# Performance work log

Measured on AMD Instinct MI355X. Metric: run time of the kernel, lower is better.

## Reference

```python
import math
import jax, jax.numpy as jnp
import numpy as np

B, N, C, H = 4, 1025, 768, 12
D = C // H                      # head_dim = 64
SCALE = D ** -0.5
NUM = N // 4                    # CSA block size = 256
FUSE_T = math.ceil(0.1 * (N - 1))     # 103
ENH_T = math.ceil(0.1 * (N - 1))      # 103


def _csa_mask():
    # has_cls=True: tokens 1..4*NUM get block id 0..3; cls (idx 0) gets -1 (unmasked).
    bid = (jnp.arange(N) - 1) // NUM
    same = (bid[:, None] == bid[None, :]) & (bid[:, None] >= 0) & (bid[:, None] < 4)
    return jnp.where(same, -jnp.inf, 0.0).astype(jnp.float32)  # [N, N]


def setup_inputs() -> dict:
    key = jax.random.key(0)
    kx, kq, kw, kb = jax.random.split(key, 4)
    x = jax.random.normal(kx, (B, N, C), dtype=jnp.float32)
    w_qkv = jax.random.normal(kq, (3 * C, C), dtype=jnp.float32) * 0.02  # Linear(C, 3C, bias=False)
    w_out = jax.random.normal(kw, (C, C), dtype=jnp.float32) * 0.02
    b_out = jax.random.normal(kb, (C,), dtype=jnp.float32) * 0.02
    return {"x": x, "w_qkv": w_qkv, "w_out": w_out, "b_out": b_out}


def reference(x, w_qkv, w_out, b_out):
    b, n, c = x.shape
    h, d = H, c // H
    # qkv projection + rearrange 'b n (qkv h d) -> qkv b h n d'
    qkv = (x @ w_qkv.T).reshape(b, n, 3, h, d).transpose(2, 0, 3, 1, 4)
    q, k, v = qkv[0], qkv[1], qkv[2]          # each [b, h, n, d]

    scores = jnp.einsum('bhxd,bhyd->bhxy', q, k) * SCALE + _csa_mask()
    att = jax.nn.softmax(scores, axis=-1)     # [b, h, n, n]  (dropout=0, eval)

    ctx = jnp.einsum('bhxy,bhyd->bhxd', att, v)
    out = ctx.transpose(0, 2, 1, 3).reshape(b, n, c) @ w_out.T + b_out

    # cls-attention-driven token selection
    cls_attn = att[:, :, 0, 1:].mean(axis=1)  # [b, n-1]
    _, fuse_idx = jax.lax.top_k(-cls_attn, FUSE_T)   # smallest, ascending
    _, enh_idx = jax.lax.top_k(cls_attn, ENH_T)      # largest, descending
    fuse_index = jnp.broadcast_to(fuse_idx[:, :, None], (b, FUSE_T, c))
    enhance_index = jnp.broadcast_to(enh_idx[:, :, None], (b, ENH_T, c))
    return (out, enhance_index, enh_idx, fuse_index, fuse_idx, cls_attn)
```

## Files before the change

kernel.cpp:

```cpp
#include <hip/hip_runtime.h>


#define B_  4
#define N_  1025
#define C_  768
#define H_  12
#define D_  64
#define M_TOT (B_ * N_)
#define M_PAD 4224
#define KEXP 2304
#define NPAD 1088

#define OFF_EIND 3148800
#define OFF_EIDX 3465216
#define OFF_FIND 3465628
#define OFF_FIDX 3782044
#define OFF_CLS  3782456

#define WS_F64   0
#define WS_XS    196608
#define WS_QKVB  5062656
#define WS_OUTB  7716864
#define WS_QE    8601600
#define WS_KE    11943936
#define WS_VT    15286272

#define DQ0 0
#define DMS 3072
#define DLG 39936
#define DMX 89136
#define DZ  89184
#define DMV 89232

#define SPLIT_A_ITEMS (M_PAD * 192)
#define SPLIT_B1_ITEMS (2304 * 192)
#define SPLIT_B2_ITEMS (768 * 192)
#define SPLIT_TOTAL (SPLIT_A_ITEMS + SPLIT_B1_ITEMS + SPLIT_B2_ITEMS)
#define SPLIT_BLOCKS ((SPLIT_TOTAL + 255) / 256)

typedef short s16x8 __attribute__((ext_vector_type(8)));
typedef float f32x4 __attribute__((ext_vector_type(4)));

__device__ inline unsigned short f2bf(float f) {
    unsigned u = __float_as_uint(f);
    u += 0x7FFF + ((u >> 16) & 1);
    return (unsigned short)(u >> 16);
}
__device__ inline float bf2f(unsigned short h) {
    return __uint_as_float(((unsigned)h) << 16);
}

__device__ __forceinline__ void gl2lds16(const unsigned short* g, unsigned short* l) {
    __builtin_amdgcn_global_load_lds(
        (const __attribute__((address_space(1))) unsigned int*)g,
        (__attribute__((address_space(3))) unsigned int*)l,
        16, 0, 0);
}

__device__ inline void gemm_decode(int lid, int NT, int& m, int& n) {
    int gi = lid / (8 * NT);
    int r  = lid % (8 * NT);
    int base = gi * 8;
    int gsize = (33 - base < 8) ? (33 - base) : 8;
    n = r / gsize;
    m = base + r % gsize;
}

__global__ __launch_bounds__(256) void fused_split_q0_kernel(
    const float* __restrict__ x, const float* __restrict__ w_qkv,
    const float* __restrict__ w_out,
    unsigned short* __restrict__ xs, unsigned short* __restrict__ qkvB,
    unsigned short* __restrict__ outB, double* __restrict__ dws)
{
    if (blockIdx.x >= SPLIT_BLOCKS) {
        const int t = threadIdx.x;
        const int wg = (blockIdx.x - SPLIT_BLOCKS) * 4 + (t >> 6);
        const int lane = t & 63;
        const int b = wg / 768, rem = wg - b * 768;
        const float* x0 = x + (size_t)b * N_ * C_;
        const float* wr = w_qkv + (size_t)rem * C_;
        double s = 0.0;
        #pragma unroll
        for (int i = 0; i < 12; i++) {
            int c = lane + i*64;
            s += (double)x0[c] * (double)wr[c];
        }
        #pragma unroll
        for (int o = 1; o < 64; o <<= 1) s += __shfl_xor(s, o);
        if (lane == 0) dws[DQ0 + wg] = s * 0.125;
        return;
    }
    int idx = blockIdx.x * 256 + threadIdx.x;
    if (idx < SPLIT_A_ITEMS) {
        int m = idx / 192, c4 = (idx - m * 192) * 4;
        ushort4 hi = make_ushort4(0,0,0,0), lo = hi;
        if (m < M_TOT) {
            float4 f = *(const float4*)&x[(size_t)m * C_ + c4];
            hi.x = f2bf(f.x); hi.y = f2bf(f.y); hi.z = f2bf(f.z); hi.w = f2bf(f.w);
            lo.x = f2bf(f.x - bf2f(hi.x)); lo.y = f2bf(f.y - bf2f(hi.y));
            lo.z = f2bf(f.z - bf2f(hi.z)); lo.w = f2bf(f.w - bf2f(hi.w));
        }
        unsigned short* d = xs + (size_t)m * KEXP + c4;
        *(ushort4*)(d)        = hi;
        *(ushort4*)(d + 768)  = hi;
        *(ushort4*)(d + 1536) = lo;
        return;
    }
    idx -= SPLIT_A_ITEMS;
    const float* src;
    unsigned short* dst;
    if (idx < SPLIT_B1_ITEMS) { src = w_qkv; dst = qkvB; }
    else { idx -= SPLIT_B1_ITEMS; if (idx >= SPLIT_B2_ITEMS) return; src = w_out; dst = outB; }
    int m = idx / 192, c4 = (idx - m * 192) * 4;
    float4 f = *(const float4*)&src[(size_t)m * C_ + c4];
    ushort4 hi, lo;
    hi.x = f2bf(f.x); hi.y = f2bf(f.y); hi.z = f2bf(f.z); hi.w = f2bf(f.w);
    lo.x = f2bf(f.x - bf2f(hi.x)); lo.y = f2bf(f.y - bf2f(hi.y));
    lo.z = f2bf(f.z - bf2f(hi.z)); lo.w = f2bf(f.w - bf2f(hi.w));
    unsigned short* d = dst + (size_t)m * KEXP + c4;
    *(ushort4*)(d)        = hi;
    *(ushort4*)(d + 768)  = lo;
    *(ushort4*)(d + 1536) = hi;
}

__global__ __launch_bounds__(256) void fused_gemm_qkv_ms_kernel(
    const unsigned short* __restrict__ A, const unsigned short* __restrict__ Bm,
    unsigned short* __restrict__ qe, unsigned short* __restrict__ ke,
    unsigned short* __restrict__ vtp,
    const float* __restrict__ w_qkv, double* __restrict__ dws)
{
    __shared__ unsigned short AsF[3*4096];
    __shared__ unsigned short BsF[3*4096];

    if (blockIdx.x >= 594) {
        double* q0s = (double*)AsF;
        const int lid = blockIdx.x - 594;
        const int cb = lid % 3;
        const int h  = (lid / 3) % 12;
        const int b  = lid / 36;
        const int t = threadIdx.x;
        const int c = cb * 256 + t;
        if (t < 64) q0s[t] = dws[DQ0 + (b*H_ + h)*64 + t];
        __syncthreads();
        const float* wk = w_qkv + (size_t)(C_ + h*64) * C_ + c;
        double s = 0.0;
        #pragma unroll 8
        for (int d = 0; d < 64; d++) s += q0s[d] * (double)wk[(size_t)d * C_];
        dws[DMS + ((size_t)(b*H_ + h))*768 + c] = s;
        return;
    }

    int mi, ni;
    gemm_decode(blockIdx.x, 18, mi, ni);
    const int n0 = ni * 128;
    const int m0 = mi * 128;
    const int t = threadIdx.x;
    const int lane = t & 63, wv = t >> 6;
    const int wr = wv >> 1, wc = wv & 1;
    const int q4 = lane >> 4, r = lane & 15;
    const int lrr = lane >> 2;
    const int lcc = ((lane & 3) ^ ((lane >> 3) & 3)) * 8;
    const int sw  = (q4 ^ ((r >> 1) & 3)) * 8;

    f32x4 acc[4][4];
    #pragma unroll
    for (int i = 0; i < 4; i++)
        #pragma unroll
        for (int j = 0; j < 4; j++)
            #pragma unroll
            for (int e = 0; e < 4; e++) acc[i][j][e] = 0.f;

    const unsigned short* gA = A  + (size_t)(m0 + wv*16 + lrr) * KEXP + lcc;
    const unsigned short* gB = Bm + (size_t)(n0 + wv*16 + lrr) * KEXP + lcc;

    auto STAGE = [&](int kt, int o) {
        const unsigned short* a = gA + kt * 32;
        const unsigned short* b = gB + kt * 32;
        gl2lds16(a,                       AsF + o + wv*512);
        gl2lds16(a + (size_t)64 * KEXP,   AsF + o + 2048 + wv*512);
        gl2lds16(b,                       BsF + o + wv*512);
        gl2lds16(b + (size_t)64 * KEXP,   BsF + o + 2048 + wv*512);
    };

    STAGE(0, 0);
    STAGE(1, 4096);

    int cb = 0;
    for (int it = 0; it < 72; ++it) {
        if (it + 1 < 72) asm volatile("s_waitcnt vmcnt(4)" ::: "memory");
        else             asm volatile("s_waitcnt vmcnt(0)" ::: "memory");
        __builtin_amdgcn_s_barrier();
        asm volatile("" ::: "memory");
        __builtin_amdgcn_sched_barrier(0);
        if (it + 2 < 72) {
            int nb = (cb >= 1) ? cb - 1 : cb + 2;
            STAGE(it + 2, nb * 4096);
        }
        const int cbuf = cb * 4096;
        s16x8 af[4], bfr[4];
        #pragma unroll
        for (int i = 0; i < 4; i++) {
            af[i]  = *(const s16x8*)&AsF[cbuf + (wr*64 + i*16 + r)*32 + sw];
            bfr[i] = *(const s16x8*)&BsF[cbuf + (wc*64 + i*16 + r)*32 + sw];
        }
        #pragma unroll
        for (int i = 0; i < 4; i++)
            #pragma unroll
            for (int j = 0; j < 4; j++)
                acc[i][j] = __builtin_amdgcn_mfma_f32_16x16x32_bf16(af[i], bfr[j], acc[i][j], 0, 0, 0);
        cb = (cb < 2) ? cb + 1 : 0;
    }

    const int sel = n0 / C_;
    const int off = n0 % C_;
    const float scl = (sel == 0) ? 0.125f : 1.0f;
    #pragma unroll
    for (int i = 0; i < 4; i++) {
        #pragma unroll
        for (int rr = 0; rr < 4; rr++) {
            int gm = m0 + wr*64 + i*16 + q4*4 + rr;
            if (gm < M_TOT) {
                int bb = gm / N_, n = gm - bb * N_;
                #pragma unroll
                for (int j = 0; j < 4; j++) {
                    int col = off + wc*64 + j*16 + r;
                    int h = col >> 6, d = col & 63;
                    float val = acc[i][j][rr] * scl;
                    unsigned short hi = f2bf(val);
                    unsigned short lo = f2bf(val - bf2f(hi));
                    size_t bh = (size_t)(bb*H_ + h);
                    if (sel <= 1) {
                        unsigned short* dst = (sel == 0 ? qe : ke) + (bh*NPAD + n)*128;
                        dst[d]      = hi;
                        dst[64 + d] = lo;
                    } else {
                        unsigned short* dst = vtp + bh*128*NPAD;
                        dst[(size_t)d*NPAD + n]        = hi;
                        dst[(size_t)(64 + d)*NPAD + n] = lo;
                    }
                }
            }
        }
    }
}

__global__ __launch_bounds__(256, 4) void fused_attn_logits_kernel(
    const unsigned short* __restrict__ qe, const unsigned short* __restrict__ ke,
    const unsigned short* __restrict__ vtp, unsigned short* __restrict__ ctxs,
    const float* __restrict__ x, double* __restrict__ dws)
{
    __shared__ unsigned short KP[64*128];
    __shared__ unsigned short VP[128*64];

    if (blockIdx.x >= 816) {
        double* xsd = (double*)KP;
        const int lid = blockIdx.x - 816;
        const int j = lid % 1025, b = lid / 1025;
        const int t = threadIdx.x;
        const int w = t >> 6, lane = t & 63;
        const float* xr = x + ((size_t)b * N_ + j) * C_;
        for (int c = t; c < C_; c += 256) xsd[c] = (double)xr[c];
        __syncthreads();
        for (int hh = 0; hh < 3; hh++) {
            int h = w + hh * 4;
            const double* ms = dws + DMS + ((size_t)(b*H_ + h))*768;
            double s = 0.0;
            #pragma unroll
            for (int i = 0; i < 12; i++) {
                int c = lane + i*64;
                s += xsd[c] * ms[c];
            }
            #pragma unroll
            for (int o = 1; o < 64; o <<= 1) s += __shfl_xor(s, o);
            if (lane == 0) dws[DLG + ((size_t)(b*H_ + h))*1025 + j] = s;
        }
        return;
    }

    const int qt = blockIdx.x / 48;
    const int g  = blockIdx.x - qt * 48;
    const int h = g % 12, b = g / 12;
    const int t = threadIdx.x;
    const int w = t >> 6, lane = t & 63;
    const int quad = lane >> 4, r16 = lane & 15;
    const size_t bh = (size_t)(b*H_ + h);

    s16x8 ah0, ah1, al0, al1;
    {
        const unsigned short* qrow = qe + (bh*NPAD + qt*64 + w*16 + r16) * 128;
        const int q8 = quad * 8;
        ah0 = *(const s16x8*)(qrow + q8);
        ah1 = *(const s16x8*)(qrow + 32 + q8);
        al0 = *(const s16x8*)(qrow + 64 + q8);
        al1 = *(const s16x8*)(qrow + 96 + q8);
    }

    int qu;
    {
        int rlo = qt*64, rhi = min(qt*64 + 63, N_ - 1);
        if (rlo == 0) qu = -2;
        else { int b1 = (rlo-1)>>8, b2 = (rhi-1)>>8; qu = (b1==b2) ? b1 : -2; }
    }

    float m_run[4], l_run[4];
    f32x4 ctx[4];
    #pragma unroll
    for (int i = 0; i < 4; i++) {
        m_run[i] = -1e30f; l_run[i] = 0.f;
        #pragma unroll
        for (int e = 0; e < 4; e++) ctx[i][e] = 0.f;
    }

    const unsigned short* keb = ke  + (bh*NPAD) * 128;
    const unsigned short* vtb = vtp + bh*(size_t)128*NPAD;

    const int kchunk = (t & 15) ^ ((t >> 4) & 15);
    const int vchunk = (t & 7)  ^ ((t >> 3) & 7);
    const unsigned short* kg0 = keb + (size_t)(t >> 4) * 128 + kchunk * 8;
    const unsigned short* vg0 = vtb + (size_t)(t >> 3) * NPAD + vchunk * 8;

    const int s0 = (quad ^ r16) << 3;
    const int sv = (quad ^ (r16 & 7)) << 3;
    unsigned short* Pew = KP + w*16*128;

    for (int kt = 0; kt < 17; kt++) {
        if (qu >= 0 && kt > 0) {
            int clo = kt*64, chi = min(kt*64 + 63, N_ - 1);
            int b1 = (clo-1)>>8, b2 = (chi-1)>>8;
            if (b1 == b2 && b1 == qu) continue;
        }

        __syncthreads();
        {
            const unsigned short* kg = kg0 + (size_t)kt * 64 * 128;
            const unsigned short* vg = vg0 + kt * 64;
            #pragma unroll
            for (int i = 0; i < 4; i++) {
                gl2lds16(kg + i * 2048,              KP + i*2048 + w*512);
                gl2lds16(vg + (size_t)i * 32 * NPAD, VP + i*2048 + w*512);
            }
        }
        __syncthreads();

        f32x4 st[4];
        #pragma unroll
        for (int j = 0; j < 4; j++)
            #pragma unroll
            for (int e = 0; e < 4; e++) st[j][e] = 0.f;
        #pragma unroll
        for (int j = 0; j < 4; j++) {
            const unsigned short* kr = &KP[(j*16 + r16) * 128];
            s16x8 bh0 = *(const s16x8*)&kr[s0];
            s16x8 bh1 = *(const s16x8*)&kr[s0 ^ 32];
            s16x8 bl0 = *(const s16x8*)&kr[s0 ^ 64];
            s16x8 bl1 = *(const s16x8*)&kr[s0 ^ 96];
            st[j] = __builtin_amdgcn_mfma_f32_16x16x32_bf16(ah0, bh0, st[j], 0,0,0);
            st[j] = __builtin_amdgcn_mfma_f32_16x16x32_bf16(ah1, bh1, st[j], 0,0,0);
            st[j] = __builtin_amdgcn_mfma_f32_16x16x32_bf16(ah0, bl0, st[j], 0,0,0);
            st[j] = __builtin_amdgcn_mfma_f32_16x16x32_bf16(ah1, bl1, st[j], 0,0,0);
            st[j] = __builtin_amdgcn_mfma_f32_16x16x32_bf16(al0, bh0, st[j], 0,0,0);
            st[j] = __builtin_amdgcn_mfma_f32_16x16x32_bf16(al1, bh1, st[j], 0,0,0);
        }

        float pv[4][4];
        float alpha[4];
        #pragma unroll
        for (int reg = 0; reg < 4; reg++) {
            int gr = qt*64 + w*16 + quad*4 + reg;
            int qb = (gr >= 1) ? ((gr - 1) >> 8) : -1;
            float mx = -1e30f;
            float vv[4];
            #pragma unroll
            for (int j = 0; j < 4; j++) {
                int gc = kt*64 + j*16 + r16;
                bool ok = (gr < N_) && (gc < N_) &&
                          !((gr >= 1) && (gc >= 1) && (((gc - 1) >> 8) == qb));
                vv[j] = ok ? st[j][reg] : -1e30f;
                mx = fmaxf(mx, vv[j]);
            }
            mx = fmaxf(mx, __shfl_xor(mx, 1));
            mx = fmaxf(mx, __shfl_xor(mx, 2));
            mx = fmaxf(mx, __shfl_xor(mx, 4));
            mx = fmaxf(mx, __shfl_xor(mx, 8));
            float mnew = fmaxf(m_run[reg], mx);
            alpha[reg] = __expf(m_run[reg] - mnew);
            m_run[reg] = mnew;
            float ps = 0.f;
            #pragma unroll
            for (int j = 0; j < 4; j++) {
                float pp = (vv[j] > -1e29f) ? __expf(vv[j] - mnew) : 0.f;
                pv[reg][j] = pp; ps += pp;
            }
            ps += __shfl_xor(ps, 1);
            ps += __shfl_xor(ps, 2);
            ps += __shfl_xor(ps, 4);
            ps += __shfl_xor(ps, 8);
            l_run[reg] = l_run[reg] * alpha[reg] + ps;
        }

        __syncthreads();

        #pragma unroll
        for (int reg = 0; reg < 4; reg++) {
            int lrow = quad*4 + reg;
            #pragma unroll
            for (int j = 0; j < 4; j++) {
                float pp = pv[reg][j];
                unsigned short ph = f2bf(pp);
                unsigned short pl = f2bf(pp - bf2f(ph));
                int colh = j*16 + r16;
                int coll = 64 + colh;
                Pew[lrow*128 + (((colh >> 3) ^ lrow) << 3) + (colh & 7)] = ph;
                Pew[lrow*128 + (((coll >> 3) ^ lrow) << 3) + (coll & 7)] = pl;
            }
        }

        #pragma unroll
        for (int nj = 0; nj < 4; nj++)
            #pragma unroll
            for (int reg = 0; reg < 4; reg++)
                ctx[nj][reg] *= alpha[reg];

        {
            const unsigned short* pr = &Pew[r16 * 128];
            s16x8 ph0 = *(const s16x8*)&pr[s0];
            s16x8 ph1 = *(const s16x8*)&pr[s0 ^ 32];
            s16x8 pl0 = *(const s16x8*)&pr[s0 ^ 64];
            s16x8 pl1 = *(const s16x8*)&pr[s0 ^ 96];
            #pragma unroll
            for (int nj = 0; nj < 4; nj++) {
                const unsigned short* vh = &VP[(nj*16 + r16) * 64];
                const unsigned short* vl = &VP[(64 + nj*16 + r16) * 64];
                s16x8 vh0 = *(const s16x8*)&vh[sv];
                s16x8 vh1 = *(const s16x8*)&vh[sv ^ 32];
                s16x8 vl0 = *(const s16x8*)&vl[sv];
                s16x8 vl1 = *(const s16x8*)&vl[sv ^ 32];
                ctx[nj] = __builtin_amdgcn_mfma_f32_16x16x32_bf16(ph0, vh0, ctx[nj], 0,0,0);
                ctx[nj] = __builtin_amdgcn_mfma_f32_16x16x32_bf16(ph1, vh1, ctx[nj], 0,0,0);
                ctx[nj] = __builtin_amdgcn_mfma_f32_16x16x32_bf16(ph0, vl0, ctx[nj], 0,0,0);
                ctx[nj] = __builtin_amdgcn_mfma_f32_16x16x32_bf16(ph1, vl1, ctx[nj], 0,0,0);
                ctx[nj] = __builtin_amdgcn_mfma_f32_16x16x32_bf16(pl0, vh0, ctx[nj], 0,0,0);
                ctx[nj] = __builtin_amdgcn_mfma_f32_16x16x32_bf16(pl1, vh1, ctx[nj], 0,0,0);
            }
        }
    }

    #pragma unroll
    for (int reg = 0; reg < 4; reg++) {
        int gr = qt*64 + w*16 + quad*4 + reg;
        if (gr < N_) {
            float inv = 1.0f / l_run[reg];
            size_t row = (size_t)(b*N_ + gr) * KEXP;
            #pragma unroll
            for (int nj = 0; nj < 4; nj++) {
                float val = ctx[nj][reg] * inv;
                unsigned short hi = f2bf(val);
                unsigned short lo = f2bf(val - bf2f(hi));
                int c = h*64 + nj*16 + r16;
                ctxs[row + c]        = hi;
                ctxs[row + 768 + c]  = hi;
                ctxs[row + 1536 + c] = lo;
            }
        }
    }
}

__global__ __launch_bounds__(256) void fused_gemm_out_reduce_kernel(
    const unsigned short* __restrict__ A, const unsigned short* __restrict__ Bm,
    const float* __restrict__ bias, float* __restrict__ out,
    double* __restrict__ dws)
{
    __shared__ unsigned short AsF[3*4096];
    __shared__ unsigned short BsF[3*4096];

    if (blockIdx.x >= 198) {
        double* red = (double*)AsF;
        const int lid = blockIdx.x - 198;
        const int h = lid % 12, b = lid / 12;
        const int t = threadIdx.x;
        const double* lg = dws + DLG + ((size_t)(b*H_ + h))*1025;
        double mloc = -1e300;
        for (int j = t; j < N_; j += 256) mloc = fmax(mloc, lg[j]);
        red[t] = mloc; __syncthreads();
        for (int o = 128; o > 0; o >>= 1) {
            if (t < o) red[t] = fmax(red[t], red[t+o]);
            __syncthreads();
        }
        double mx = red[0]; __syncthreads();
        double sloc = 0.0;
        for (int j = t; j < N_; j += 256) sloc += exp(lg[j] - mx);
        red[t] = sloc; __syncthreads();
        for (int o = 128; o > 0; o >>= 1) {
            if (t < o) red[t] += red[t+o];
            __syncthreads();
        }
        if (t == 0) {
            dws[DMX + b*H_ + h] = mx;
            dws[DZ  + b*H_ + h] = red[0];
        }
        return;
    }

    int mi, ni;
    gemm_decode(blockIdx.x, 6, mi, ni);
    const int n0 = ni * 128;
    const int m0 = mi * 128;
    const int t = threadIdx.x;
    const int lane = t & 63, wv = t >> 6;
    const int wr = wv >> 1, wc = wv & 1;
    const int q4 = lane >> 4, r = lane & 15;
    const int lrr = lane >> 2;
    const int lcc = ((lane & 3) ^ ((lane >> 3) & 3)) * 8;
    const int sw  = (q4 ^ ((r >> 1) & 3)) * 8;

    f32x4 acc[4][4];
    #pragma unroll
    for (int i = 0; i < 4; i++)
        #pragma unroll
        for (int j = 0; j < 4; j++)
            #pragma unroll
            for (int e = 0; e < 4; e++) acc[i][j][e] = 0.f;

    const unsigned short* gA = A  + (size_t)(m0 + wv*16 + lrr) * KEXP + lcc;
    const unsigned short* gB = Bm + (size_t)(n0 + wv*16 + lrr) * KEXP + lcc;

    auto STAGE = [&](int kt, int o) {
        const unsigned short* a = gA + kt * 32;
        const unsigned short* b = gB + kt * 32;
        gl2lds16(a,                       AsF + o + wv*512);
        gl2lds16(a + (size_t)64 * KEXP,   AsF + o + 2048 + wv*512);
        gl2lds16(b,                       BsF + o + wv*512);
        gl2lds16(b + (size_t)64 * KEXP,   BsF + o + 2048 + wv*512);
    };

    STAGE(0, 0);
    STAGE(1, 4096);

    int cb = 0;
    for (int it = 0; it < 72; ++it) {
        if (it + 1 < 72) asm volatile("s_waitcnt vmcnt(4)" ::: "memory");
        else             asm volatile("s_waitcnt vmcnt(0)" ::: "memory");
        __builtin_amdgcn_s_barrier();
        asm volatile("" ::: "memory");
        __builtin_amdgcn_sched_barrier(0);
        if (it + 2 < 72) {
            int nb = (cb >= 1) ? cb - 1 : cb + 2;
            STAGE(it + 2, nb * 4096);
        }
        const int cbuf = cb * 4096;
        s16x8 af[4], bfr[4];
        #pragma unroll
        for (int i = 0; i < 4; i++) {
            af[i]  = *(const s16x8*)&AsF[cbuf + (wr*64 + i*16 + r)*32 + sw];
            bfr[i] = *(const s16x8*)&BsF[cbuf + (wc*64 + i*16 + r)*32 + sw];
        }
        #pragma unroll
        for (int i = 0; i < 4; i++)
            #pragma unroll
            for (int j = 0; j < 4; j++)
                acc[i][j] = __builtin_amdgcn_mfma_f32_16x16x32_bf16(af[i], bfr[j], acc[i][j], 0, 0, 0);
        cb = (cb < 2) ? cb + 1 : 0;
    }

    #pragma unroll
    for (int i = 0; i < 4; i++) {
        #pragma unroll
        for (int rr = 0; rr < 4; rr++) {
            int gm = m0 + wr*64 + i*16 + q4*4 + rr;
            if (gm < M_TOT) {
                #pragma unroll
                for (int j = 0; j < 4; j++) {
                    int col = n0 + wc*64 + j*16 + r;
                    out[(size_t)gm * C_ + col] = acc[i][j][rr] + bias[col];
                }
            }
        }
    }
}

__global__ __launch_bounds__(256) void cls_score_kernel(
    const double* __restrict__ dwsr, double* __restrict__ dws,
    float* __restrict__ out)
{
    const int idx = blockIdx.x * 256 + threadIdx.x;
    const int b = idx >> 10, t = idx & 1023;
    double s = 0.0;
    #pragma unroll
    for (int h = 0; h < H_; h++) {
        double mx = dwsr[DMX + b*H_ + h];
        double Z  = dwsr[DZ  + b*H_ + h];
        double lg = dwsr[DLG + ((size_t)(b*H_ + h))*1025 + (t + 1)];
        s += exp(lg - mx) / Z;
    }
    s *= (1.0 / 12.0);
    dws[DMV + idx] = s;
    out[OFF_CLS + (size_t)b*1024 + t] = (float)s;
}

__global__ __launch_bounds__(256) void cls_rank_kernel(
    const double* __restrict__ dws, float* __restrict__ out)
{
    __shared__ double mv[1024];
    const int q = blockIdx.x, b = blockIdx.y;
    const int tid = threadIdx.x;
    for (int i = tid; i < 1024; i += 256) mv[i] = dws[DMV + b*1024 + i];
    __syncthreads();
    const int t = q*256 + tid;
    const double v = mv[t];
    int cd = 0, ca = 0;
    #pragma unroll 8
    for (int j = 0; j < 1024; j++) {
        double u = mv[j];
        bool tie = (u == v) && (j < t);
        cd += (u > v) || tie;
        ca += (u < v) || tie;
    }
    if (cd < 103) out[OFF_EIDX + (size_t)b*103 + cd] = (float)t;
    if (ca < 103) out[OFF_FIDX + (size_t)b*103 + ca] = (float)t;
}

__global__ __launch_bounds__(256) void cls_fill_kernel(float* __restrict__ out)
{
    const int PER = 103 * 192;
    int idx = blockIdx.x * 256 + threadIdx.x;
    if (idx >= 2 * 4 * PER) return;
    int sel = idx / (4 * PER);
    int r   = idx - sel * 4 * PER;
    int b   = r / PER;
    int rem = r - b * PER;
    int e   = rem / 192;
    int c4  = (rem - e * 192) * 4;
    float val = out[(sel ? OFF_FIDX : OFF_EIDX) + (size_t)b*103 + e];
    float* dst = out + (sel ? OFF_FIND : OFF_EIND) + ((size_t)b*103 + e)*768 + c4;
    *(float4*)dst = make_float4(val, val, val, val);
}

extern "C" void kernel_launch(void* const* d_in, const int* in_sizes, int n_in,
                              void* d_out, int out_size, void* d_ws, size_t ws_size,
                              hipStream_t stream)
{
    const float* x     = (const float*)d_in[0];
    const float* w_qkv = (const float*)d_in[1];
    const float* w_out = (const float*)d_in[2];
    const float* b_out = (const float*)d_in[3];
    float* out = (float*)d_out;
    float* ws  = (float*)d_ws;

    double* dws = (double*)(ws + WS_F64);
    unsigned short* xs   = (unsigned short*)(ws + WS_XS);
    unsigned short* qkvB = (unsigned short*)(ws + WS_QKVB);
    unsigned short* outB = (unsigned short*)(ws + WS_OUTB);
    unsigned short* qe   = (unsigned short*)(ws + WS_QE);
    unsigned short* ke   = (unsigned short*)(ws + WS_KE);
    unsigned short* vtp  = (unsigned short*)(ws + WS_VT);

    fused_split_q0_kernel<<<SPLIT_BLOCKS + 768, 256, 0, stream>>>(
        x, w_qkv, w_out, xs, qkvB, outB, dws);

    fused_gemm_qkv_ms_kernel<<<594 + 144, 256, 0, stream>>>(
        xs, qkvB, qe, ke, vtp, w_qkv, dws);

    fused_attn_logits_kernel<<<816 + 4100, 256, 0, stream>>>(
        qe, ke, vtp, xs, x, dws);

    fused_gemm_out_reduce_kernel<<<198 + 48, 256, 0, stream>>>(
        xs, outB, b_out, out, dws);

    cls_score_kernel<<<16, 256, 0, stream>>>(dws, dws, out);
    cls_rank_kernel<<<dim3(4, B_), 256, 0, stream>>>(dws, out);
    cls_fill_kernel<<<618, 256, 0, stream>>>(out);
}
```

Measured before the change: 348.9 us.

## Shrink GEMM M-tile to 64 rows and raise MFMA wave priority in attention

Both bf16-split GEMMs (QKV projection and output projection) now use 64x128 tiles instead of 128x128, with all four waves sharing the A rows and each owning 32 columns. This doubles the block count and cuts LDS per block, with launch_bounds set to allow 4 blocks per CU. The goal is better CU fill for the small out-projection grid, which had 198 blocks. In the attention kernel, s_setprio raises wave priority around the MFMA loops to favour matrix issue. The cost is lower data reuse per tile and more redundant B-tile loads.

```diff
diff --git a/kernel.cpp b/kernel.cpp
--- a/kernel.cpp
+++ b/kernel.cpp
@@ -38,6 +38,12 @@
 #define SPLIT_TOTAL (SPLIT_A_ITEMS + SPLIT_B1_ITEMS + SPLIT_B2_ITEMS)
 #define SPLIT_BLOCKS ((SPLIT_TOTAL + 255) / 256)
 
+#define QKV_MT 66
+#define QKV_NT 18
+#define QKV_BLOCKS (QKV_MT * QKV_NT)
+#define OUT_NT 6
+#define OUT_BLOCKS (QKV_MT * OUT_NT)
+
 typedef short s16x8 __attribute__((ext_vector_type(8)));
 typedef float f32x4 __attribute__((ext_vector_type(4)));
 
@@ -57,11 +63,11 @@
         16, 0, 0);
 }
 
-__device__ inline void gemm_decode(int lid, int NT, int& m, int& n) {
+__device__ inline void gemm_decode2(int lid, int MT, int NT, int& m, int& n) {
     int gi = lid / (8 * NT);
     int r  = lid % (8 * NT);
     int base = gi * 8;
-    int gsize = (33 - base < 8) ? (33 - base) : 8;
+    int gsize = (MT - base < 8) ? (MT - base) : 8;
     n = r / gsize;
     m = base + r % gsize;
 }
@@ -123,18 +129,18 @@
     *(ushort4*)(d + 1536) = hi;
 }
 
-__global__ __launch_bounds__(256) void fused_gemm_qkv_ms_kernel(
+__global__ __launch_bounds__(256, 4) void fused_gemm_qkv_ms_kernel(
     const unsigned short* __restrict__ A, const unsigned short* __restrict__ Bm,
     unsigned short* __restrict__ qe, unsigned short* __restrict__ ke,
     unsigned short* __restrict__ vtp,
     const float* __restrict__ w_qkv, double* __restrict__ dws)
 {
-    __shared__ unsigned short AsF[3*4096];
+    __shared__ unsigned short AsF[3*2048];
     __shared__ unsigned short BsF[3*4096];
 
-    if (blockIdx.x >= 594) {
+    if (blockIdx.x >= QKV_BLOCKS) {
         double* q0s = (double*)AsF;
-        const int lid = blockIdx.x - 594;
+        const int lid = blockIdx.x - QKV_BLOCKS;
         const int cb = lid % 3;
         const int h  = (lid / 3) % 12;
         const int b  = lid / 36;
@@ -151,62 +157,61 @@
     }
 
     int mi, ni;
-    gemm_decode(blockIdx.x, 18, mi, ni);
+    gemm_decode2(blockIdx.x, QKV_MT, QKV_NT, mi, ni);
     const int n0 = ni * 128;
-    const int m0 = mi * 128;
+    const int m0 = mi * 64;
     const int t = threadIdx.x;
     const int lane = t & 63, wv = t >> 6;
-    const int wr = wv >> 1, wc = wv & 1;
     const int q4 = lane >> 4, r = lane & 15;
     const int lrr = lane >> 2;
     const int lcc = ((lane & 3) ^ ((lane >> 3) & 3)) * 8;
     const int sw  = (q4 ^ ((r >> 1) & 3)) * 8;
 
-    f32x4 acc[4][4];
+    f32x4 acc[4][2];
     #pragma unroll
     for (int i = 0; i < 4; i++)
         #pragma unroll
-        for (int j = 0; j < 4; j++)
+        for (int j = 0; j < 2; j++)
             #pragma unroll
             for (int e = 0; e < 4; e++) acc[i][j][e] = 0.f;
 
     const unsigned short* gA = A  + (size_t)(m0 + wv*16 + lrr) * KEXP + lcc;
     const unsigned short* gB = Bm + (size_t)(n0 + wv*16 + lrr) * KEXP + lcc;
 
-    auto STAGE = [&](int kt, int o) {
+    auto STAGE = [&](int kt, int buf) {
         const unsigned short* a = gA + kt * 32;
         const unsigned short* b = gB + kt * 32;
-        gl2lds16(a,                       AsF + o + wv*512);
-        gl2lds16(a + (size_t)64 * KEXP,   AsF + o + 2048 + wv*512);
-        gl2lds16(b,                       BsF + o + wv*512);
-        gl2lds16(b + (size_t)64 * KEXP,   BsF + o + 2048 + wv*512);
+        gl2lds16(a,                       AsF + buf*2048 + wv*512);
+        gl2lds16(b,                       BsF + buf*4096 + wv*512);
+        gl2lds16(b + (size_t)64 * KEXP,   BsF + buf*4096 + 2048 + wv*512);
     };
 
     STAGE(0, 0);
-    STAGE(1, 4096);
+    STAGE(1, 1);
 
     int cb = 0;
     for (int it = 0; it < 72; ++it) {
-        if (it + 1 < 72) asm volatile("s_waitcnt vmcnt(4)" ::: "memory");
+        if (it + 1 < 72) asm volatile("s_waitcnt vmcnt(3)" ::: "memory");
         else             asm volatile("s_waitcnt vmcnt(0)" ::: "memory");
         __builtin_amdgcn_s_barrier();
         asm volatile("" ::: "memory");
         __builtin_amdgcn_sched_barrier(0);
         if (it + 2 < 72) {
             int nb = (cb >= 1) ? cb - 1 : cb + 2;
-            STAGE(it + 2, nb * 4096);
-        }
-        const int cbuf = cb * 4096;
-        s16x8 af[4], bfr[4];
-        #pragma unroll
-        for (int i = 0; i < 4; i++) {
-            af[i]  = *(const s16x8*)&AsF[cbuf + (wr*64 + i*16 + r)*32 + sw];
-            bfr[i] = *(const s16x8*)&BsF[cbuf + (wc*64 + i*16 + r)*32 + sw];
-        }
+            STAGE(it + 2, nb);
+        }
+        const int cA = cb * 2048, cB = cb * 4096;
+        s16x8 af[4], bfr[2];
         #pragma unroll
         for (int i = 0; i < 4; i++)
-            #pragma unroll
-            for (int j = 0; j < 4; j++)
+            af[i]  = *(const s16x8*)&AsF[cA + (i*16 + r)*32 + sw];
+        #pragma unroll
+        for (int j = 0; j < 2; j++)
+            bfr[j] = *(const s16x8*)&BsF[cB + (wv*32 + j*16 + r)*32 + sw];
+        #pragma unroll
+        for (int i = 0; i < 4; i++)
+            #pragma unroll
+            for (int j = 0; j < 2; j++)
                 acc[i][j] = __builtin_amdgcn_mfma_f32_16x16x32_bf16(af[i], bfr[j], acc[i][j], 0, 0, 0);
         cb = (cb < 2) ? cb + 1 : 0;
     }
@@ -218,12 +223,12 @@
     for (int i = 0; i < 4; i++) {
         #pragma unroll
         for (int rr = 0; rr < 4; rr++) {
-            int gm = m0 + wr*64 + i*16 + q4*4 + rr;
+            int gm = m0 + i*16 + q4*4 + rr;
             if (gm < M_TOT) {
                 int bb = gm / N_, n = gm - bb * N_;
                 #pragma unroll
-                for (int j = 0; j < 4; j++) {
-                    int col = off + wc*64 + j*16 + r;
+                for (int j = 0; j < 2; j++) {
+                    int col = off + wv*32 + j*16 + r;
                     int h = col >> 6, d = col & 63;
                     float val = acc[i][j][rr] * scl;
                     unsigned short hi = f2bf(val);
@@ -347,6 +352,7 @@
         for (int j = 0; j < 4; j++)
             #pragma unroll
             for (int e = 0; e < 4; e++) st[j][e] = 0.f;
+        __builtin_amdgcn_s_setprio(1);
         #pragma unroll
         for (int j = 0; j < 4; j++) {
             const unsigned short* kr = &KP[(j*16 + r16) * 128];
@@ -361,6 +367,7 @@
             st[j] = __builtin_amdgcn_mfma_f32_16x16x32_bf16(al0, bh0, st[j], 0,0,0);
             st[j] = __builtin_amdgcn_mfma_f32_16x16x32_bf16(al1, bh1, st[j], 0,0,0);
         }
+        __builtin_amdgcn_s_setprio(0);
 
         float pv[4][4];
         float alpha[4];
@@ -427,6 +434,7 @@
             s16x8 ph1 = *(const s16x8*)&pr[s0 ^ 32];
             s16x8 pl0 = *(const s16x8*)&pr[s0 ^ 64];
             s16x8 pl1 = *(const s16x8*)&pr[s0 ^ 96];
+            __builtin_amdgcn_s_setprio(1);
             #pragma unroll
             for (int nj = 0; nj < 4; nj++) {
                 const unsigned short* vh = &VP[(nj*16 + r16) * 64];
@@ -442,6 +450,7 @@
                 ctx[nj] = __builtin_amdgcn_mfma_f32_16x16x32_bf16(pl0, vh0, ctx[nj], 0,0,0);
                 ctx[nj] = __builtin_amdgcn_mfma_f32_16x16x32_bf16(pl1, vh1, ctx[nj], 0,0,0);
             }
+            __builtin_amdgcn_s_setprio(0);
         }
     }
 
@@ -465,17 +474,17 @@
     }
 }
 
-__global__ __launch_bounds__(256) void fused_gemm_out_reduce_kernel(
+__global__ __launch_bounds__(256, 4) void fused_gemm_out_reduce_kernel(
     const unsigned short* __restrict__ A, const unsigned short* __restrict__ Bm,
     const float* __restrict__ bias, float* __restrict__ out,
     double* __restrict__ dws)
 {
-    __shared__ unsigned short AsF[3*4096];
+    __shared__ unsigned short AsF[3*2048];
     __shared__ unsigned short BsF[3*4096];
 
-    if (blockIdx.x >= 198) {
+    if (blockIdx.x >= OUT_BLOCKS) {
         double* red = (double*)AsF;
-        const int lid = blockIdx.x - 198;
+        const int lid = blockIdx.x - OUT_BLOCKS;
         const int h = lid % 12, b = lid / 12;
         const int t = threadIdx.x;
         const double* lg = dws + DLG + ((size_t)(b*H_ + h))*1025;
@@ -502,62 +511,61 @@
     }
 
     int mi, ni;
-    gemm_decode(blockIdx.x, 6, mi, ni);
+    gemm_decode2(blockIdx.x, QKV_MT, OUT_NT, mi, ni);
     const int n0 = ni * 128;
-    const int m0 = mi * 128;
+    const int m0 = mi * 64;
     const int t = threadIdx.x;
     const int lane = t & 63, wv = t >> 6;
-    const int wr = wv >> 1, wc = wv & 1;
     const int q4 = lane >> 4, r = lane & 15;
     const int lrr = lane >> 2;
     const int lcc = ((lane & 3) ^ ((lane >> 3) & 3)) * 8;
     const int sw  = (q4 ^ ((r >> 1) & 3)) * 8;
 
-    f32x4 acc[4][4];
+    f32x4 acc[4][2];
     #pragma unroll
     for (int i = 0; i < 4; i++)
         #pragma unroll
-        for (int j = 0; j < 4; j++)
+        for (int j = 0; j < 2; j++)
             #pragma unroll
             for (int e = 0; e < 4; e++) acc[i][j][e] = 0.f;
 
     const unsigned short* gA = A  + (size_t)(m0 + wv*16 + lrr) * KEXP + lcc;
     const unsigned short* gB = Bm + (size_t)(n0 + wv*16 + lrr) * KEXP + lcc;
 
-    auto STAGE = [&](int kt, int o) {
+    auto STAGE = [&](int kt, int buf) {
         const unsigned short* a = gA + kt * 32;
         const unsigned short* b = gB + kt * 32;
-        gl2lds16(a,                       AsF + o + wv*512);
-        gl2lds16(a + (size_t)64 * KEXP,   AsF + o + 2048 + wv*512);
-        gl2lds16(b,                       BsF + o + wv*512);
-        gl2lds16(b + (size_t)64 * KEXP,   BsF + o + 2048 + wv*512);
+        gl2lds16(a,                       AsF + buf*2048 + wv*512);
+        gl2lds16(b,                       BsF + buf*4096 + wv*512);
+        gl2lds16(b + (size_t)64 * KEXP,   BsF + buf*4096 + 2048 + wv*512);
     };
 
     STAGE(0, 0);
-    STAGE(1, 4096);
+    STAGE(1, 1);
 
     int cb = 0;
     for (int it = 0; it < 72; ++it) {
-        if (it + 1 < 72) asm volatile("s_waitcnt vmcnt(4)" ::: "memory");
+        if (it + 1 < 72) asm volatile("s_waitcnt vmcnt(3)" ::: "memory");
         else             asm volatile("s_waitcnt vmcnt(0)" ::: "memory");
         __builtin_amdgcn_s_barrier();
         asm volatile("" ::: "memory");
         __builtin_amdgcn_sched_barrier(0);
         if (it + 2 < 72) {
             int nb = (cb >= 1) ? cb - 1 : cb + 2;
-            STAGE(it + 2, nb * 4096);
-        }
-        const int cbuf = cb * 4096;
-        s16x8 af[4], bfr[4];
-        #pragma unroll
-        for (int i = 0; i < 4; i++) {
-            af[i]  = *(const s16x8*)&AsF[cbuf + (wr*64 + i*16 + r)*32 + sw];
-            bfr[i] = *(const s16x8*)&BsF[cbuf + (wc*64 + i*16 + r)*32 + sw];
-        }
+            STAGE(it + 2, nb);
+        }
+        const int cA = cb * 2048, cB = cb * 4096;
+        s16x8 af[4], bfr[2];
         #pragma unroll
         for (int i = 0; i < 4; i++)
-            #pragma unroll
-            for (int j = 0; j < 4; j++)
+            af[i]  = *(const s16x8*)&AsF[cA + (i*16 + r)*32 + sw];
+        #pragma unroll
+        for (int j = 0; j < 2; j++)
+            bfr[j] = *(const s16x8*)&BsF[cB + (wv*32 + j*16 + r)*32 + sw];
+        #pragma unroll
+        for (int i = 0; i < 4; i++)
+            #pragma unroll
+            for (int j = 0; j < 2; j++)
                 acc[i][j] = __builtin_amdgcn_mfma_f32_16x16x32_bf16(af[i], bfr[j], acc[i][j], 0, 0, 0);
         cb = (cb < 2) ? cb + 1 : 0;
     }
@@ -566,11 +574,11 @@
     for (int i = 0; i < 4; i++) {
         #pragma unroll
         for (int rr = 0; rr < 4; rr++) {
-            int gm = m0 + wr*64 + i*16 + q4*4 + rr;
+            int gm = m0 + i*16 + q4*4 + rr;
             if (gm < M_TOT) {
                 #pragma unroll
-                for (int j = 0; j < 4; j++) {
-                    int col = n0 + wc*64 + j*16 + r;
+                for (int j = 0; j < 2; j++) {
+                    int col = n0 + wv*32 + j*16 + r;
                     out[(size_t)gm * C_ + col] = acc[i][j][rr] + bias[col];
                 }
             }
@@ -657,13 +665,13 @@
     fused_split_q0_kernel<<<SPLIT_BLOCKS + 768, 256, 0, stream>>>(
         x, w_qkv, w_out, xs, qkvB, outB, dws);
 
-    fused_gemm_qkv_ms_kernel<<<594 + 144, 256, 0, stream>>>(
+    fused_gemm_qkv_ms_kernel<<<QKV_BLOCKS + 144, 256, 0, stream>>>(
         xs, qkvB, qe, ke, vtp, w_qkv, dws);
 
     fused_attn_logits_kernel<<<816 + 4100, 256, 0, stream>>>(
         qe, ke, vtp, xs, x, dws);
 
-    fused_gemm_out_reduce_kernel<<<198 + 48, 256, 0, stream>>>(
+    fused_gemm_out_reduce_kernel<<<OUT_BLOCKS + 48, 256, 0, stream>>>(
         xs, outB, b_out, out, dws);
 
     cls_score_kernel<<<16, 256, 0, stream>>>(dws, dws, out);
```

Result: slower. 362.3 us (+3.8%).
